# Kernel tuning notes

Measured on AMD Instinct MI355X. Metric: run time of the kernel, lower is better.

## Reference

```python
import jax, jax.numpy as jnp
import numpy as np

N = 16_777_216  # point count


def _skew(v):
    zero = jnp.zeros((), v.dtype)
    return jnp.stack([
        jnp.stack([zero, -v[2], v[1]]),
        jnp.stack([v[2], zero, -v[0]]),
        jnp.stack([-v[1], v[0], zero]),
    ])


def _se3_exp(tau):
    # tau = [rho(3), theta(3)]; returns (R, t) of exp(tau^)
    rho, theta = tau[:3], tau[3:]
    W = _skew(theta)
    W2 = W @ W
    angle = jnp.linalg.norm(theta)
    small = angle < 1e-5
    a = jnp.where(small, jnp.ones((), tau.dtype), angle)  # safe divisor
    I = jnp.eye(3, dtype=tau.dtype)
    A = jnp.where(small, 1.0, jnp.sin(a) / a)                    # SO3 W coeff
    B = jnp.where(small, 0.5, (1.0 - jnp.cos(a)) / (a * a))      # SO3 W2 / V W coeff
    C = jnp.where(small, 1.0 / 6.0, (a - jnp.sin(a)) / (a ** 3)) # V W2 coeff
    R = I + A * W + B * W2
    Vm = I + B * W + C * W2
    return R, Vm @ rho


def setup_inputs() -> dict:
    key = jax.random.key(0)
    kx, kr, kt, ks = jax.random.split(key, 4)
    x = jax.random.normal(kx, (N, 4), dtype=jnp.float32)
    rot_delta = 0.1 * jax.random.normal(kr, (3,), dtype=jnp.float32)
    trans_delta = 0.1 * jax.random.normal(kt, (3,), dtype=jnp.float32)
    scale = 1.0 + 0.05 * jax.random.normal(ks, (3,), dtype=jnp.float32)
    R = jnp.eye(3, dtype=jnp.float32)
    T = jnp.zeros((3,), dtype=jnp.float32)
    return {"x": x, "rot_delta": rot_delta, "trans_delta": trans_delta,
            "scale": scale, "R": R, "T": T}


def reference(x, rot_delta, trans_delta, scale, R, T):
    tau = jnp.concatenate([trans_delta, rot_delta])  # [6]
    delta_r, delta_t = _se3_exp(tau)
    top = jnp.concatenate([scale * (delta_r @ R), (T + delta_t)[:, None]], axis=1)  # [3,4]
    bottom = jnp.array([[0.0, 0.0, 0.0, 1.0]], dtype=x.dtype)
    trans = jnp.concatenate([top, bottom], axis=0)  # [4,4]
    # y = (trans @ x.T).T == x @ trans.T
    return x @ trans.T
```

## Files before the change

### kernel.cpp

```cpp
#include <hip/hip_runtime.h>
#include <math.h>

__global__ void build_trans(const float* __restrict__ rot_delta,
                            const float* __restrict__ trans_delta,
                            const float* __restrict__ scale,
                            const float* __restrict__ Rin,
                            const float* __restrict__ Tin,
                            float* __restrict__ M) {
    if (threadIdx.x != 0 || blockIdx.x != 0) return;

    const float th0 = rot_delta[0], th1 = rot_delta[1], th2 = rot_delta[2];
    const float r0 = trans_delta[0], r1 = trans_delta[1], r2 = trans_delta[2];

    const float angle = sqrtf(th0*th0 + th1*th1 + th2*th2);
    const bool small = angle < 1e-5f;
    const float a = small ? 1.0f : angle;
    const float s = sinf(a), c = cosf(a);
    const float A = small ? 1.0f        : s / a;
    const float B = small ? 0.5f        : (1.0f - c) / (a * a);
    const float C = small ? (1.0f/6.0f) : (a - s) / (a * a * a);

    float W[3][3] = {{0.0f, -th2,  th1},
                     { th2, 0.0f, -th0},
                     {-th1,  th0, 0.0f}};
    float W2[3][3];
    for (int i = 0; i < 3; ++i)
        for (int j = 0; j < 3; ++j)
            W2[i][j] = W[i][0]*W[0][j] + W[i][1]*W[1][j] + W[i][2]*W[2][j];

    float Rd[3][3], Vm[3][3];
    for (int i = 0; i < 3; ++i)
        for (int j = 0; j < 3; ++j) {
            const float I = (i == j) ? 1.0f : 0.0f;
            Rd[i][j] = I + A * W[i][j] + B * W2[i][j];
            Vm[i][j] = I + B * W[i][j] + C * W2[i][j];
        }

    const float dt0 = Vm[0][0]*r0 + Vm[0][1]*r1 + Vm[0][2]*r2;
    const float dt1 = Vm[1][0]*r0 + Vm[1][1]*r1 + Vm[1][2]*r2;
    const float dt2 = Vm[2][0]*r0 + Vm[2][1]*r1 + Vm[2][2]*r2;

    for (int i = 0; i < 3; ++i)
        for (int j = 0; j < 3; ++j) {
            const float v = Rd[i][0]*Rin[0*3+j] + Rd[i][1]*Rin[1*3+j] + Rd[i][2]*Rin[2*3+j];
            M[i*4 + j] = scale[j] * v;
        }
    M[0*4 + 3] = Tin[0] + dt0;
    M[1*4 + 3] = Tin[1] + dt1;
    M[2*4 + 3] = Tin[2] + dt2;
    M[3*4 + 0] = 0.0f; M[3*4 + 1] = 0.0f; M[3*4 + 2] = 0.0f; M[3*4 + 3] = 1.0f;
}

__global__ __launch_bounds__(256) void apply_trans(const float4* __restrict__ x,
                                                   const float* __restrict__ M,
                                                   float4* __restrict__ out,
                                                   int n) {
    const float m00 = M[0],  m01 = M[1],  m02 = M[2],  m03 = M[3];
    const float m10 = M[4],  m11 = M[5],  m12 = M[6],  m13 = M[7];
    const float m20 = M[8],  m21 = M[9],  m22 = M[10], m23 = M[11];

    const int i = blockIdx.x * blockDim.x + threadIdx.x;
    if (i >= n) return;
    const float4 v = x[i];
    float4 o;
    o.x = fmaf(m00, v.x, fmaf(m01, v.y, fmaf(m02, v.z, m03 * v.w)));
    o.y = fmaf(m10, v.x, fmaf(m11, v.y, fmaf(m12, v.z, m13 * v.w)));
    o.z = fmaf(m20, v.x, fmaf(m21, v.y, fmaf(m22, v.z, m23 * v.w)));
    o.w = v.w;
    out[i] = o;
}

extern "C" void kernel_launch(void* const* d_in, const int* in_sizes, int n_in,
                              void* d_out, int out_size, void* d_ws, size_t ws_size,
                              hipStream_t stream) {
    const float* x          = (const float*)d_in[0];
    const float* rot_delta  = (const float*)d_in[1];
    const float* trans_delta= (const float*)d_in[2];
    const float* scale      = (const float*)d_in[3];
    const float* R          = (const float*)d_in[4];
    const float* T          = (const float*)d_in[5];
    float* M = (float*)d_ws;

    build_trans<<<1, 64, 0, stream>>>(rot_delta, trans_delta, scale, R, T, M);

    const int n = in_sizes[0] / 4;
    const int block = 256;
    const int grid = (n + block - 1) / block;
    apply_trans<<<grid, block, 0, stream>>>((const float4*)x, M, (float4*)d_out, n);
}
```

Baseline: 428.3 us.

## Fuse transform build into apply kernel with grid-stride 4x unrolled loop

Removes the single-thread build_trans launch and has every thread recompute the 3x4 transform from the small parameter inputs, then applies it. The apply kernel becomes a grid-stride loop capped at 2048 blocks, with four float4 loads in flight per iteration. This drops one kernel launch and the serial dependency between the two kernels, at the cost of redundant per-thread transcendental math and fewer resident blocks.

```diff
diff --git a/kernel.cpp b/kernel.cpp
--- a/kernel.cpp
+++ b/kernel.cpp
@@ -1,14 +1,16 @@
 #include <hip/hip_runtime.h>
 #include <math.h>
 
-__global__ void build_trans(const float* __restrict__ rot_delta,
-                            const float* __restrict__ trans_delta,
-                            const float* __restrict__ scale,
-                            const float* __restrict__ Rin,
-                            const float* __restrict__ Tin,
-                            float* __restrict__ M) {
-    if (threadIdx.x != 0 || blockIdx.x != 0) return;
-
+__global__ __launch_bounds__(256) void fused_apply(
+    const float4* __restrict__ x,
+    const float* __restrict__ rot_delta,
+    const float* __restrict__ trans_delta,
+    const float* __restrict__ scale,
+    const float* __restrict__ Rin,
+    const float* __restrict__ Tin,
+    float4* __restrict__ out,
+    int n)
+{
     const float th0 = rot_delta[0], th1 = rot_delta[1], th2 = rot_delta[2];
     const float r0 = trans_delta[0], r1 = trans_delta[1], r2 = trans_delta[2];
 
@@ -20,16 +22,20 @@
     const float B = small ? 0.5f        : (1.0f - c) / (a * a);
     const float C = small ? (1.0f/6.0f) : (a - s) / (a * a * a);
 
-    float W[3][3] = {{0.0f, -th2,  th1},
-                     { th2, 0.0f, -th0},
-                     {-th1,  th0, 0.0f}};
+    const float W[3][3] = {{0.0f, -th2,  th1},
+                           { th2, 0.0f, -th0},
+                           {-th1,  th0, 0.0f}};
     float W2[3][3];
+    #pragma unroll
     for (int i = 0; i < 3; ++i)
+        #pragma unroll
         for (int j = 0; j < 3; ++j)
             W2[i][j] = W[i][0]*W[0][j] + W[i][1]*W[1][j] + W[i][2]*W[2][j];
 
     float Rd[3][3], Vm[3][3];
+    #pragma unroll
     for (int i = 0; i < 3; ++i)
+        #pragma unroll
         for (int j = 0; j < 3; ++j) {
             const float I = (i == j) ? 1.0f : 0.0f;
             Rd[i][j] = I + A * W[i][j] + B * W2[i][j];
@@ -40,51 +46,80 @@
     const float dt1 = Vm[1][0]*r0 + Vm[1][1]*r1 + Vm[1][2]*r2;
     const float dt2 = Vm[2][0]*r0 + Vm[2][1]*r1 + Vm[2][2]*r2;
 
+    float m[3][4];
+    #pragma unroll
     for (int i = 0; i < 3; ++i)
+        #pragma unroll
         for (int j = 0; j < 3; ++j) {
             const float v = Rd[i][0]*Rin[0*3+j] + Rd[i][1]*Rin[1*3+j] + Rd[i][2]*Rin[2*3+j];
-            M[i*4 + j] = scale[j] * v;
+            m[i][j] = scale[j] * v;
         }
-    M[0*4 + 3] = Tin[0] + dt0;
-    M[1*4 + 3] = Tin[1] + dt1;
-    M[2*4 + 3] = Tin[2] + dt2;
-    M[3*4 + 0] = 0.0f; M[3*4 + 1] = 0.0f; M[3*4 + 2] = 0.0f; M[3*4 + 3] = 1.0f;
-}
+    m[0][3] = Tin[0] + dt0;
+    m[1][3] = Tin[1] + dt1;
+    m[2][3] = Tin[2] + dt2;
 
-__global__ __launch_bounds__(256) void apply_trans(const float4* __restrict__ x,
-                                                   const float* __restrict__ M,
-                                                   float4* __restrict__ out,
-                                                   int n) {
-    const float m00 = M[0],  m01 = M[1],  m02 = M[2],  m03 = M[3];
-    const float m10 = M[4],  m11 = M[5],  m12 = M[6],  m13 = M[7];
-    const float m20 = M[8],  m21 = M[9],  m22 = M[10], m23 = M[11];
+    const float m00 = m[0][0], m01 = m[0][1], m02 = m[0][2], m03 = m[0][3];
+    const float m10 = m[1][0], m11 = m[1][1], m12 = m[1][2], m13 = m[1][3];
+    const float m20 = m[2][0], m21 = m[2][1], m22 = m[2][2], m23 = m[2][3];
 
-    const int i = blockIdx.x * blockDim.x + threadIdx.x;
-    if (i >= n) return;
-    const float4 v = x[i];
-    float4 o;
-    o.x = fmaf(m00, v.x, fmaf(m01, v.y, fmaf(m02, v.z, m03 * v.w)));
-    o.y = fmaf(m10, v.x, fmaf(m11, v.y, fmaf(m12, v.z, m13 * v.w)));
-    o.z = fmaf(m20, v.x, fmaf(m21, v.y, fmaf(m22, v.z, m23 * v.w)));
-    o.w = v.w;
-    out[i] = o;
+    const int stride = (int)(gridDim.x * blockDim.x);
+    int i = (int)(blockIdx.x * blockDim.x + threadIdx.x);
+
+    for (; i + 3 * stride < n; i += 4 * stride) {
+        const float4 v0 = x[i];
+        const float4 v1 = x[i + stride];
+        const float4 v2 = x[i + 2 * stride];
+        const float4 v3 = x[i + 3 * stride];
+
+        float4 o0, o1, o2, o3;
+        o0.x = fmaf(m00, v0.x, fmaf(m01, v0.y, fmaf(m02, v0.z, m03 * v0.w)));
+        o0.y = fmaf(m10, v0.x, fmaf(m11, v0.y, fmaf(m12, v0.z, m13 * v0.w)));
+        o0.z = fmaf(m20, v0.x, fmaf(m21, v0.y, fmaf(m22, v0.z, m23 * v0.w)));
+        o0.w = v0.w;
+        o1.x = fmaf(m00, v1.x, fmaf(m01, v1.y, fmaf(m02, v1.z, m03 * v1.w)));
+        o1.y = fmaf(m10, v1.x, fmaf(m11, v1.y, fmaf(m12, v1.z, m13 * v1.w)));
+        o1.z = fmaf(m20, v1.x, fmaf(m21, v1.y, fmaf(m22, v1.z, m23 * v1.w)));
+        o1.w = v1.w;
+        o2.x = fmaf(m00, v2.x, fmaf(m01, v2.y, fmaf(m02, v2.z, m03 * v2.w)));
+        o2.y = fmaf(m10, v2.x, fmaf(m11, v2.y, fmaf(m12, v2.z, m13 * v2.w)));
+        o2.z = fmaf(m20, v2.x, fmaf(m21, v2.y, fmaf(m22, v2.z, m23 * v2.w)));
+        o2.w = v2.w;
+        o3.x = fmaf(m00, v3.x, fmaf(m01, v3.y, fmaf(m02, v3.z, m03 * v3.w)));
+        o3.y = fmaf(m10, v3.x, fmaf(m11, v3.y, fmaf(m12, v3.z, m13 * v3.w)));
+        o3.z = fmaf(m20, v3.x, fmaf(m21, v3.y, fmaf(m22, v3.z, m23 * v3.w)));
+        o3.w = v3.w;
+
+        out[i]              = o0;
+        out[i + stride]     = o1;
+        out[i + 2 * stride] = o2;
+        out[i + 3 * stride] = o3;
+    }
+    for (; i < n; i += stride) {
+        const float4 v = x[i];
+        float4 o;
+        o.x = fmaf(m00, v.x, fmaf(m01, v.y, fmaf(m02, v.z, m03 * v.w)));
+        o.y = fmaf(m10, v.x, fmaf(m11, v.y, fmaf(m12, v.z, m13 * v.w)));
+        o.z = fmaf(m20, v.x, fmaf(m21, v.y, fmaf(m22, v.z, m23 * v.w)));
+        o.w = v.w;
+        out[i] = o;
+    }
 }
 
 extern "C" void kernel_launch(void* const* d_in, const int* in_sizes, int n_in,
                               void* d_out, int out_size, void* d_ws, size_t ws_size,
                               hipStream_t stream) {
-    const float* x          = (const float*)d_in[0];
-    const float* rot_delta  = (const float*)d_in[1];
-    const float* trans_delta= (const float*)d_in[2];
-    const float* scale      = (const float*)d_in[3];
-    const float* R          = (const float*)d_in[4];
-    const float* T          = (const float*)d_in[5];
-    float* M = (float*)d_ws;
-
-    build_trans<<<1, 64, 0, stream>>>(rot_delta, trans_delta, scale, R, T, M);
+    const float* x           = (const float*)d_in[0];
+    const float* rot_delta   = (const float*)d_in[1];
+    const float* trans_delta = (const float*)d_in[2];
+    const float* scale       = (const float*)d_in[3];
+    const float* R           = (const float*)d_in[4];
+    const float* T           = (const float*)d_in[5];
 
     const int n = in_sizes[0] / 4;
     const int block = 256;
-    const int grid = (n + block - 1) / block;
-    apply_trans<<<grid, block, 0, stream>>>((const float4*)x, M, (float4*)d_out, n);
+    int grid = (n + block - 1) / block;
+    if (grid > 2048) grid = 2048;
+
+    fused_apply<<<grid, block, 0, stream>>>((const float4*)x, rot_delta, trans_delta,
+                                            scale, R, T, (float4*)d_out, n);
 }
```

New measurement: 462.4 us. 1.08x slower.
